# Performance work log

Hardware: AMD Instinct MI355X
Metric: run time of the kernel (lower is better)

## Reference

```python
import jax, jax.numpy as jnp
import numpy as np

NUM_MOVIES = 100000
MOVIE_FEAT = 128
USER_FEAT = 128
BATCH = 16384
N_NBRS = 50
D0, D1, D2 = 256, 256, 128  # layer_dims


def setup_inputs() -> dict:
    key = jax.random.key(0)
    ks = jax.random.split(key, 16)
    inp = {
        "users": jax.random.normal(ks[0], (BATCH, USER_FEAT), jnp.float32),
        "pos_movies": jax.random.normal(ks[1], (BATCH, MOVIE_FEAT), jnp.float32),
        "neg_movies": jax.random.normal(ks[2], (BATCH, MOVIE_FEAT), jnp.float32),
        "user_ids": jax.random.randint(ks[3], (BATCH,), 0, BATCH),
        "pos_movie_ids": jax.random.randint(ks[4], (BATCH,), 0, NUM_MOVIES),
        "neg_movie_ids": jax.random.randint(ks[5], (BATCH,), 0, NUM_MOVIES),
        "nbr_ids": jax.random.randint(ks[6], (BATCH, N_NBRS), 0, NUM_MOVIES),
        # learned params / buffers
        "movie_table": jax.random.normal(ks[7], (NUM_MOVIES, MOVIE_FEAT), jnp.float32),
        "Wu": jax.random.normal(ks[8], (USER_FEAT, D0), jnp.float32) * (1.0 / np.sqrt(USER_FEAT)),
        "bu": jnp.zeros((D0,), jnp.float32),
        "Wm": jax.random.normal(ks[9], (MOVIE_FEAT, D0), jnp.float32) * (1.0 / np.sqrt(MOVIE_FEAT)),
        "bm": jnp.zeros((D0,), jnp.float32),
        "W1": jax.random.normal(ks[10], (D0, D1), jnp.float32) * (1.0 / np.sqrt(D0)),
        "b1": jnp.zeros((D1,), jnp.float32),
        "W2": jax.random.normal(ks[11], (D1, D2), jnp.float32) * (1.0 / np.sqrt(D1)),
        "b2": jnp.zeros((D2,), jnp.float32),
    }
    return inp


def reference(users, pos_movies, neg_movies, user_ids, pos_movie_ids, neg_movie_ids,
              nbr_ids, movie_table, Wu, bu, Wm, bm, W1, b1, W2, b2):
    # user_projection / movie_projection
    user_emb = users @ Wu + bu                      # [B, D0]
    movie_emb = movie_table @ Wm + bm               # [N, D0]
    pos_emb = movie_emb[pos_movie_ids]              # [B, D0]
    neg_emb = movie_emb[neg_movie_ids]              # [B, D0]
    # vectorized replacement of the per-user neighbor gather + mean loop
    nbr_mean = jnp.mean(movie_emb[nbr_ids], axis=1)  # [B, N_NBRS, D0] -> [B, D0]
    user_emb = user_emb + nbr_mean
    x = jnp.stack([user_emb, pos_emb, neg_emb], axis=0)  # [3, B, D0]
    x = jax.nn.relu(x @ W1 + b1)
    x = jax.nn.relu(x @ W2 + b2)
    return (x[0], x[1], x[2])
```

## Files before the change

### kernel.cpp

```cpp
#include <hip/hip_runtime.h>
#include <hip/hip_bf16.h>

#define BATCH_N   16384
#define FEAT      128
#define NNBR      50
#define NUM_MOVIES_N 100000

typedef short  short8  __attribute__((ext_vector_type(8)));
typedef float  floatx4 __attribute__((ext_vector_type(4)));
typedef unsigned int u32;

__device__ __forceinline__ __hip_bfloat16 f2bf(float x) { return __float2bfloat16(x); }
__device__ __forceinline__ float bfb2f(short s) {
  union { u32 u; float f; } c; c.u = ((u32)(unsigned short)s) << 16; return c.f;
}

__device__ __forceinline__ void gld16(const __hip_bfloat16* g, __hip_bfloat16* l) {
  __builtin_amdgcn_global_load_lds(
      (const __attribute__((address_space(1))) u32*)g,
      (__attribute__((address_space(3))) u32*)l, 16, 0, 0);
}

__device__ __forceinline__ floatx4 mfma16(short8 a, short8 b, floatx4 c) {
  return __builtin_amdgcn_mfma_f32_16x16x32_bf16(a, b, c, 0, 0, 0);
}

#define CONV_BLOCKS (NUM_MOVIES_N * FEAT / (256 * 8))
__global__ __launch_bounds__(256) void prep_all(
    const float* __restrict__ t, __hip_bfloat16* __restrict__ tb,
    const float* __restrict__ Wu, const float* __restrict__ Wm,
    const float* __restrict__ W1, const float* __restrict__ W2,
    const float* __restrict__ bu, const float* __restrict__ bm,
    __hip_bfloat16* __restrict__ WcatT, __hip_bfloat16* __restrict__ WmT,
    __hip_bfloat16* __restrict__ W1T,  __hip_bfloat16* __restrict__ W2T,
    float* __restrict__ bc) {
  int bid = blockIdx.x;
  if (bid < CONV_BLOCKS) {
    size_t i = ((size_t)bid * 256 + threadIdx.x) * 8;
    float4 v0 = *(const float4*)(t + i);
    float4 v1 = *(const float4*)(t + i + 4);
    __hip_bfloat16 o[8];
    o[0] = f2bf(v0.x); o[1] = f2bf(v0.y); o[2] = f2bf(v0.z); o[3] = f2bf(v0.w);
    o[4] = f2bf(v1.x); o[5] = f2bf(v1.y); o[6] = f2bf(v1.z); o[7] = f2bf(v1.w);
    *(short8*)(tb + i) = *(short8*)o;
  } else {
    int idx = (bid - CONV_BLOCKS) * 256 + threadIdx.x;
    int n = idx & 255, k = idx >> 8;
    float v = (k < 128) ? Wu[k * 256 + n] : Wm[(k - 128) * 256 + n];
    WcatT[n * 256 + k] = f2bf(v);
    W1T[n * 256 + k]   = f2bf(W1[k * 256 + n]);
    if (k < 128) WmT[n * 128 + k] = f2bf(Wm[k * 256 + n]);
    if (idx < 32768) {
      int k2 = idx >> 7, n2 = idx & 127;
      W2T[n2 * 256 + k2] = f2bf(W2[k2 * 128 + n2]);
    }
    if (idx < 256) bc[idx] = bu[idx] + bm[idx];
  }
}

template <int K0, int NCOL, bool RELU, bool TOGLB>
__device__ __forceinline__ void layer(
    const __hip_bfloat16* Ain,
    const __hip_bfloat16* __restrict__ Wt, const float* __restrict__ bias,
    __hip_bfloat16* Olds, float* __restrict__ Oglb,
    int wid, int quad, int lrow) {
  constexpr int KK = K0 / 32;
  constexpr int JN = NCOL / 128;
  const int c0 = wid * JN * 16;

  short8 bfr[JN][KK];
  float  bv[JN];
  #pragma unroll
  for (int j = 0; j < JN; ++j) {
    #pragma unroll
    for (int kc = 0; kc < KK; ++kc)
      bfr[j][kc] = *(const short8*)(Wt + (size_t)(c0 + j * 16 + lrow) * K0 +
                                    kc * 32 + quad * 8);
    bv[j] = bias[c0 + j * 16 + lrow];
  }

  #pragma unroll
  for (int it = 0; it < 4; ++it) {
    int r = it * 16 + lrow;
    short8 af[KK];
    #pragma unroll
    for (int kc = 0; kc < KK; ++kc)
      af[kc] = *(const short8*)&Ain[r * K0 + (((kc * 4 + quad) ^ (r & 7)) << 3)];
    floatx4 pa[JN], pb[JN];
    #pragma unroll
    for (int j = 0; j < JN; ++j) { pa[j] = {}; pb[j] = {}; }
    #pragma unroll
    for (int kc = 0; kc < KK; kc += 2)
      #pragma unroll
      for (int j = 0; j < JN; ++j) {
        pa[j] = mfma16(af[kc],     bfr[j][kc],     pa[j]);
        pb[j] = mfma16(af[kc + 1], bfr[j][kc + 1], pb[j]);
      }
    #pragma unroll
    for (int j = 0; j < JN; ++j) {
      floatx4 a = pa[j] + pb[j];
      int col = c0 + j * 16 + lrow;
      #pragma unroll
      for (int rr = 0; rr < 4; ++rr) {
        int row = it * 16 + quad * 4 + rr;
        float v = a[rr] + bv[j];
        if (RELU) v = fmaxf(v, 0.f);
        if (TOGLB) {
          Oglb[(size_t)row * NCOL + col] = v;
        } else {
          int ch = col >> 3;
          Olds[row * 256 + (((ch ^ (row & 7)) << 3) | (col & 7))] = f2bf(v);
        }
      }
    }
  }
}

__global__ __launch_bounds__(512)
__attribute__((amdgpu_waves_per_eu(2, 2)))
void fused_mlp(
    const float* __restrict__ users,
    const __hip_bfloat16* __restrict__ tb,
    const int* __restrict__ pos_ids, const int* __restrict__ neg_ids,
    const int* __restrict__ nbr_ids,
    const __hip_bfloat16* __restrict__ WcatT,
    const __hip_bfloat16* __restrict__ WmT,
    const __hip_bfloat16* __restrict__ W1T,
    const __hip_bfloat16* __restrict__ W2T,
    const float* __restrict__ bc, const float* __restrict__ bmv,
    const float* __restrict__ b1, const float* __restrict__ b2,
    float* __restrict__ out) {
  __shared__ __hip_bfloat16 A_lds[64 * 256];
  __shared__ __hip_bfloat16 E_lds[64 * 256];

  const int t    = threadIdx.x;
  const int lane = t & 63, wid = t >> 6;
  const int quad = lane >> 4, lrow = lane & 15;

  int s, tile;
  if (blockIdx.x < 256) { s = 0; tile = blockIdx.x; }
  else { int k = blockIdx.x - 256; s = 1 + (k & 1); tile = k >> 1; }
  const long m0 = (long)tile * 64;

  if (s == 0) {
    for (int rr = 0; rr < 8; ++rr) {
      const int r = (wid << 3) | rr;
      const size_t grow = (size_t)(m0 + r);
      const int* nb = nbr_ids + grow * NNBR;
      float acc[8] = {0.f, 0.f, 0.f, 0.f, 0.f, 0.f, 0.f, 0.f};
      #pragma unroll
      for (int it = 0; it < 13; ++it) {
        int j = (it << 2) + quad;
        if (j < NNBR) {
          int id = nb[j];
          short8 v = *(const short8*)(tb + (size_t)id * FEAT + (lrow << 3));
          #pragma unroll
          for (int e = 0; e < 8; ++e) acc[e] += bfb2f(v[e]);
        }
      }
      __hip_bfloat16 o[8];
      #pragma unroll
      for (int e = 0; e < 8; ++e) {
        float v = acc[e];
        v += __shfl_xor(v, 16, 64);
        v += __shfl_xor(v, 32, 64);
        o[e] = f2bf(v * (1.f / NNBR));
      }
      if (quad == 0) {
        int ch = 16 + lrow;
        *(short8*)(A_lds + r * 256 + ((ch ^ (r & 7)) << 3)) = *(short8*)o;
      }
      float2 uv = ((const float2*)(users + grow * FEAT))[lane];
      __hip_bfloat162 t0; t0.x = f2bf(uv.x); t0.y = f2bf(uv.y);
      int col = lane << 1, ch2 = col >> 3;
      *(__hip_bfloat162*)(A_lds + r * 256 + ((ch2 ^ (r & 7)) << 3) + (col & 7)) = t0;
    }
  } else {
    const int* ids = (s == 1) ? pos_ids : neg_ids;
    #pragma unroll
    for (int i = 0; i < 2; ++i) {
      int c = t + i * 512;
      int r = c >> 4, sl = c & 15;
      int id = ids[m0 + r];
      gld16(tb + ((size_t)id << 7) + ((sl ^ (r & 7)) << 3),
            A_lds + (c << 3));
    }
  }
  __syncthreads();

  if (s == 0)
    layer<256, 256, false, false>(A_lds, WcatT, bc, E_lds, nullptr,
                                  wid, quad, lrow);
  else
    layer<128, 256, false, false>(A_lds, WmT, bmv, E_lds, nullptr,
                                  wid, quad, lrow);
  __syncthreads();

  layer<256, 256, true, false>(E_lds, W1T, b1, A_lds, nullptr,
                               wid, quad, lrow);
  __syncthreads();

  layer<256, 128, true, true>(A_lds, W2T, b2, nullptr,
                              out + ((size_t)s * BATCH_N + m0) * 128,
                              wid, quad, lrow);
}

extern "C" void kernel_launch(void* const* d_in, const int* in_sizes, int n_in,
                              void* d_out, int out_size, void* d_ws, size_t ws_size,
                              hipStream_t stream) {
  const float* users   = (const float*)d_in[0];
  const int*   pos_ids = (const int*)d_in[4];
  const int*   neg_ids = (const int*)d_in[5];
  const int*   nbr_ids = (const int*)d_in[6];
  const float* table   = (const float*)d_in[7];
  const float* Wu = (const float*)d_in[8];
  const float* bu = (const float*)d_in[9];
  const float* Wm = (const float*)d_in[10];
  const float* bm = (const float*)d_in[11];
  const float* W1 = (const float*)d_in[12];
  const float* b1 = (const float*)d_in[13];
  const float* W2 = (const float*)d_in[14];
  const float* b2 = (const float*)d_in[15];
  float* out = (float*)d_out;

  char* p = (char*)d_ws;
  auto carve = [&](size_t bytes) { char* r = p; p += (bytes + 255) & ~(size_t)255; return r; };
  __hip_bfloat16* tb     = (__hip_bfloat16*)carve((size_t)NUM_MOVIES_N * FEAT * 2);
  __hip_bfloat16* WcatT  = (__hip_bfloat16*)carve(256 * 256 * 2);
  __hip_bfloat16* WmT    = (__hip_bfloat16*)carve(256 * 128 * 2);
  __hip_bfloat16* W1T    = (__hip_bfloat16*)carve(256 * 256 * 2);
  __hip_bfloat16* W2T    = (__hip_bfloat16*)carve(128 * 256 * 2);
  float*          bc     = (float*)carve(256 * 4);

  prep_all<<<CONV_BLOCKS + 256, 256, 0, stream>>>(
      table, tb, Wu, Wm, W1, W2, bu, bm, WcatT, WmT, W1T, W2T, bc);
  fused_mlp<<<3 * BATCH_N / 64, 512, 0, stream>>>(
      users, tb, pos_ids, neg_ids, nbr_ids, WcatT, WmT, W1T, W2T,
      bc, bm, b1, b2, out);
}
```

Baseline: 199.2 us.

## Pipeline neighbor gather through LDS with async loads and prefetched ids

Each wave in the user-path blocks now preloads all 400 of its neighbor ids into registers and all eight of its user feature rows up front. The neighbor embedding rows are then gathered with asynchronous global-to-LDS loads into a double-buffered staging area in E_lds, using explicit vmcnt waits so the next chunk is in flight while the current one is summed. The aim is to hide gather latency that was exposed by the previous dependent id-load then row-load chain. In exchange it adds shuffle work to hand out ids, raises register pressure, and relies on hand-counted waitcnt correctness.

```diff
diff --git a/kernel.cpp b/kernel.cpp
--- a/kernel.cpp
+++ b/kernel.cpp
@@ -24,6 +24,9 @@
 __device__ __forceinline__ floatx4 mfma16(short8 a, short8 b, floatx4 c) {
   return __builtin_amdgcn_mfma_f32_16x16x32_bf16(a, b, c, 0, 0, 0);
 }
+
+#define WAITVM2 asm volatile("s_waitcnt vmcnt(2)" ::: "memory")
+#define WAITVM0 asm volatile("s_waitcnt vmcnt(0)" ::: "memory")
 
 #define CONV_BLOCKS (NUM_MOVIES_N * FEAT / (256 * 8))
 __global__ __launch_bounds__(256) void prep_all(
@@ -143,37 +146,77 @@
   const long m0 = (long)tile * 64;
 
   if (s == 0) {
-    for (int rr = 0; rr < 8; ++rr) {
-      const int r = (wid << 3) | rr;
-      const size_t grow = (size_t)(m0 + r);
-      const int* nb = nbr_ids + grow * NNBR;
-      float acc[8] = {0.f, 0.f, 0.f, 0.f, 0.f, 0.f, 0.f, 0.f};
-      #pragma unroll
-      for (int it = 0; it < 13; ++it) {
-        int j = (it << 2) + quad;
-        if (j < NNBR) {
-          int id = nb[j];
-          short8 v = *(const short8*)(tb + (size_t)id * FEAT + (lrow << 3));
-          #pragma unroll
-          for (int e = 0; e < 8; ++e) acc[e] += bfb2f(v[e]);
+    const int rbase = wid << 3;
+    const int* nbw = nbr_ids + (size_t)(m0 + rbase) * NNBR;
+    int idreg[7];
+    #pragma unroll
+    for (int w = 0; w < 7; ++w) {
+      int fl = w * 64 + lane;
+      idreg[w] = nbw[fl < 8 * NNBR ? fl : 8 * NNBR - 1];
+    }
+    float2 uvr[8];
+    #pragma unroll
+    for (int r = 0; r < 8; ++r)
+      uvr[r] = ((const float2*)(users + (size_t)(m0 + rbase + r) * FEAT))[lane];
+
+    __hip_bfloat16* stg = E_lds + (wid << 11);
+
+    auto getid = [&](int fb) -> int {
+      int idx = fb + quad;
+      int v = __shfl(idreg[fb >> 6], idx & 63, 64);
+      if ((fb >> 6) != ((fb + 3) >> 6)) {
+        int v2 = __shfl(idreg[(fb + 3) >> 6], idx & 63, 64);
+        v = ((idx >> 6) == (fb >> 6)) ? v : v2;
+      }
+      return v;
+    };
+    auto issue = [&](int k) {
+      int row = k / 7, c = k % 7;
+      int id0 = getid(row * NNBR + c * 8);
+      int id1 = getid(row * NNBR + c * 8 + 4);
+      __hip_bfloat16* dst = stg + ((k & 1) << 10);
+      gld16(tb + (size_t)id0 * FEAT + (lrow << 3), dst + (lane << 3));
+      gld16(tb + (size_t)id1 * FEAT + (lrow << 3), dst + 512 + (lane << 3));
+    };
+
+    issue(0); issue(1);
+    float acc[8] = {0.f, 0.f, 0.f, 0.f, 0.f, 0.f, 0.f, 0.f};
+    #pragma unroll
+    for (int k = 0; k < 56; ++k) {
+      if (k < 55) { WAITVM2; } else { WAITVM0; }
+      const __hip_bfloat16* b = stg + ((k & 1) << 10);
+      int c = k % 7;
+      short8 x0 = *(const short8*)(b + (lane << 3));
+      if (c < 6) {
+        short8 x1 = *(const short8*)(b + 512 + (lane << 3));
+        #pragma unroll
+        for (int e = 0; e < 8; ++e) { acc[e] += bfb2f(x0[e]); acc[e] += bfb2f(x1[e]); }
+      } else if (quad < 2) {
+        #pragma unroll
+        for (int e = 0; e < 8; ++e) acc[e] += bfb2f(x0[e]);
+      }
+      if (c == 6) {
+        int row = k / 7, r = rbase + row;
+        __hip_bfloat16 o[8];
+        #pragma unroll
+        for (int e = 0; e < 8; ++e) {
+          float v = acc[e];
+          v += __shfl_xor(v, 16, 64);
+          v += __shfl_xor(v, 32, 64);
+          o[e] = f2bf(v * (1.f / NNBR));
+          acc[e] = 0.f;
         }
-      }
-      __hip_bfloat16 o[8];
-      #pragma unroll
-      for (int e = 0; e < 8; ++e) {
-        float v = acc[e];
-        v += __shfl_xor(v, 16, 64);
-        v += __shfl_xor(v, 32, 64);
-        o[e] = f2bf(v * (1.f / NNBR));
-      }
-      if (quad == 0) {
-        int ch = 16 + lrow;
-        *(short8*)(A_lds + r * 256 + ((ch ^ (r & 7)) << 3)) = *(short8*)o;
-      }
-      float2 uv = ((const float2*)(users + grow * FEAT))[lane];
-      __hip_bfloat162 t0; t0.x = f2bf(uv.x); t0.y = f2bf(uv.y);
-      int col = lane << 1, ch2 = col >> 3;
-      *(__hip_bfloat162*)(A_lds + r * 256 + ((ch2 ^ (r & 7)) << 3) + (col & 7)) = t0;
+        if (quad == 0) {
+          int ch = 16 + lrow;
+          *(short8*)(A_lds + r * 256 + ((ch ^ (r & 7)) << 3)) = *(short8*)o;
+        }
+        float2 uv = uvr[row];
+        __hip_bfloat162 t0; t0.x = f2bf(uv.x); t0.y = f2bf(uv.y);
+        int col = lane << 1, ch2 = col >> 3;
+        *(__hip_bfloat162*)(A_lds + r * 256 + ((ch2 ^ (r & 7)) << 3) + (col & 7)) = t0;
+      }
+      __builtin_amdgcn_sched_barrier(0);
+      if (k + 2 < 56) issue(k + 2);
     }
   } else {
     const int* ids = (s == 1) ? pos_ids : neg_ids;
```

Result: faster. 193.4 us (-2.9%).
